# Kernel tuning notes

Measured on AMD Instinct MI355X. Metric: run time of the kernel, lower is better.

The kernel has to match this reference:

```python
import jax, jax.numpy as jnp
import numpy as np

N, F_IN, PRE, K = 400000, 64, 32, 6
EDGE = [32, 32]


def _dense_params(key, fan_in, fan_out):
    kw, kb = jax.random.split(key)
    W = jax.random.normal(kw, (fan_in, fan_out), jnp.float32) / np.sqrt(fan_in).astype(np.float32)
    b = jnp.zeros((fan_out,), jnp.float32)
    return W, b


def setup_inputs() -> dict:
    key = jax.random.key(0)
    ks = jax.random.split(key, 10)
    x = jax.random.normal(ks[0], (N, F_IN), jnp.float32)
    distsq = jax.random.uniform(ks[1], (N, K), jnp.float32)
    nidx = jax.random.randint(ks[2], (N, K), 0, N, jnp.int64)
    Wp, bp = _dense_params(ks[3], F_IN, PRE)
    # edge MLP: input K*(PRE+1) -> 32 -> 32 -> K
    We1, be1 = _dense_params(ks[4], K * (PRE + 1), EDGE[0])
    We2, be2 = _dense_params(ks[5], EDGE[0], EDGE[1])
    We3, be3 = _dense_params(ks[6], EDGE[1], K)
    # self MLP: F_IN -> 32 -> 32 -> 1
    Ws1, bs1 = _dense_params(ks[7], F_IN, EDGE[0])
    Ws2, bs2 = _dense_params(ks[8], EDGE[0], EDGE[1])
    Ws3, bs3 = _dense_params(ks[9], EDGE[1], 1)
    return dict(x=x, distsq=distsq, nidx=nidx, Wp=Wp, bp=bp,
                We1=We1, be1=be1, We2=We2, be2=be2, We3=We3, be3=be3,
                Ws1=Ws1, bs1=bs1, Ws2=Ws2, bs2=bs2, Ws3=Ws3, bs3=bs3)


def _forward(x, distsq, nidx, Wp, bp, We1, be1, We2, be2, We3, be3,
             Ws1, bs1, Ws2, bs2, Ws3, bs3):
    # pre-dense: [N, PRE]
    x_p = jax.nn.elu(x @ Wp + bp)
    # gather neighbors; select(nidx, x_n, 0.0) masks nidx<0 to 0.0
    safe_idx = jnp.maximum(nidx, 0)
    gathered = x_p[safe_idx]                              # [N, K, PRE]
    gathered = jnp.where(nidx[:, :, None] < 0, 0.0, gathered)
    diff = x_p[:, None, :] - gathered                     # [N, K, PRE]
    xn = jnp.concatenate([diff, distsq[:, :, None]], axis=2)  # [N, K, PRE+1]
    xn = xn.reshape(xn.shape[0], K * (PRE + 1))
    xn = jax.nn.elu(xn @ We1 + be1)
    xn = jax.nn.elu(xn @ We2 + be2)
    xn = xn @ We3 + be3                                   # [N, K]
    xs = jax.nn.elu(x @ Ws1 + bs1)
    xs = jax.nn.elu(xs @ Ws2 + bs2)
    xs = xs @ Ws3 + bs3                                   # [N, 1]
    out = jnp.concatenate([xs, xn], axis=1)               # [N, K+1]
    return jax.nn.softmax(out, axis=1)


def reference(x, distsq, nidx, Wp, bp, We1, be1, We2, be2, We3, be3,
              Ws1, bs1, Ws2, bs2, Ws3, bs3):
    return _forward(x, distsq, nidx, Wp, bp, We1, be1, We2, be2, We3, be3,
                    Ws1, bs1, Ws2, bs2, Ws3, bs3)
```

## Files before the change

kernel.cpp:

```cpp
#include <hip/hip_runtime.h>
#include <hip/hip_bf16.h>
#include <math.h>

typedef __hip_bfloat16 bf16;
typedef __attribute__((ext_vector_type(8))) __bf16 bf16x8;
typedef __attribute__((ext_vector_type(4))) float f32x4;
typedef unsigned int u32x4 __attribute__((ext_vector_type(4)));

#define F_IN 64
#define KNB 6

#define WOFF_BP   2048
#define WOFF_BE2  9472
#define WOFF_BE3  9696
#define WOFF_BS1  11776
#define WOFF_BS2  12832
#define WOFF_BS3  12896
#define FLAGS_OFF 13056
#define FRAG_OFF  14592
#define NFRAG_PRE 11
#define NFRAG_EDGE 19
#define STAGE_OFF 24576

#define MFMA(a, b, c) __builtin_amdgcn_mfma_f32_16x16x32_bf16(a, b, c, 0, 0, 0)

__device__ __forceinline__ float b2f(bf16 v) { return __bfloat162float(v); }
__device__ __forceinline__ float eluf(float v) { return v > 0.f ? v : __expf(v) - 1.f; }

__device__ __forceinline__ ushort f2bu(float v) {
  __bf16 b = (__bf16)v; ushort u; __builtin_memcpy(&u, &b, 2); return u;
}

union U8 { uint4 u; bf16x8 v; ushort s[8]; };

__device__ __forceinline__ uint4 ntload16(const void* p) {
  u32x4 t = __builtin_nontemporal_load((const u32x4*)p);
  uint4 r; r.x = t.x; r.y = t.y; r.z = t.z; r.w = t.w; return r;
}

__device__ __forceinline__ bf16x8 ldfrag(const ushort* fr, int f) {
  U8 u; u.u = *(const uint4*)(fr + f * 512 + (threadIdx.x & 63) * 8);
  return u.v;
}

__device__ __forceinline__ int permo(int m, int t) { return 8 * (m >> 2) + (m & 3) + 4 * t; }

__global__ void setupK(const ushort* xb, const int* ni,
                       const void* Wp, const void* bp, const void* We1, const void* be1,
                       const void* We2, const void* be2, const void* We3, const void* be3,
                       const void* Ws1, const void* bs1, const void* Ws2, const void* bs2,
                       const void* Ws3, const void* bs3, float* w) {
  __shared__ int sbf;
  int t = threadIdx.x;
  if (t < 64) {
    int bad = 0;
    for (int i = t; i < 256; i += 64) {
      float v = __uint_as_float(((unsigned)xb[i]) << 16);
      if (!(fabsf(v) < 100.f)) bad++;
    }
    unsigned long long bm = __ballot(bad > 0);
    if (t == 0) sbf = (__popcll(bm) < 4) ? 1 : 0;
  }
  __syncthreads();
  int bf = sbf;
  auto rv = [&](const void* p, long i) -> float {
    return bf ? b2f(((const bf16*)p)[i]) : ((const float*)p)[i];
  };
  if (blockIdx.x == 0) {
    if (t < 64) {
      unsigned long long hm = __ballot(ni[2 * t + 1] != 0);
      if (t == 0) {
        ((int*)(w + FLAGS_OFF))[0] = bf;
        ((int*)(w + FLAGS_OFF))[1] = (hm == 0ULL) ? 1 : 0;
      }
    }
    const void* bsrc[6] = {bp, bs1, bs2, bs3, be2, be3};
    const int bn[6] = {32, 32, 32, 1, 32, 6};
    const int bo[6] = {WOFF_BP, WOFF_BS1, WOFF_BS2, WOFF_BS3, WOFF_BE2, WOFF_BE3};
    for (int a = 0; a < 6; a++)
      for (int i = t; i < bn[a]; i += blockDim.x)
        w[bo[a] + i] = rv(bsrc[a], i);
  }
  ushort* fbv = (ushort*)(w + FRAG_OFF);
  int total = (NFRAG_PRE + NFRAG_EDGE) * 512;
  for (int i = blockIdx.x * blockDim.x + t; i < total; i += gridDim.x * blockDim.x) {
    int f = i >> 9, e = i & 511;
    int lane = e >> 3, j = e & 7;
    int mm = lane & 15, qq = lane >> 4;
    int k = qq * 8 + j;
    float v = 0.f;
    if (f < 4) { int s = f >> 1, tt = f & 1; v = rv(Wp, (long)(32 * s + k) * 32 + permo(mm, tt)); }
    else if (f < 8) { int s = (f - 4) >> 1, tt = f & 1; v = rv(Ws1, (long)(32 * s + k) * 32 + permo(mm, tt)); }
    else if (f < 10) { int tt = f & 1; v = rv(Ws2, (long)k * 32 + permo(mm, tt)); }
    else if (f == 10) { v = (mm == 0) ? rv(Ws3, k) : 0.f; }
    else if (f < 23) { int kn = (f - 11) >> 1, tt = (f - 11) & 1;
                       v = -rv(We1, (long)(kn * 33 + k) * 32 + permo(mm, tt)); }
    else if (f < 25) { int tt = f - 23; float s = 0.f;
#pragma unroll
                       for (int kn = 0; kn < KNB; kn++)
                         s += rv(We1, (long)(kn * 33 + k) * 32 + permo(mm, tt));
                       v = s; }
    else if (f < 27) { int tt = f - 25; int o = permo(mm, tt);
                       v = (k < 6) ? rv(We1, (long)(k * 33 + 32) * 32 + o)
                                   : (k == 6 ? rv(be1, o) : 0.f); }
    else if (f < 29) { int tt = f - 27; v = rv(We2, (long)k * 32 + permo(mm, tt)); }
    else { v = (mm < KNB) ? rv(We3, (long)k * 6 + mm) : 0.f; }
    fbv[i] = f2bu(v);
  }
}

template <bool BF16>
__device__ void pre_tiles(const void* xv, const float* __restrict__ w,
                          ushort* __restrict__ xp, float* __restrict__ xs,
                          int n_nodes, const ushort* __restrict__ fr) {
  int lane = threadIdx.x & 63;
  int m = lane & 15, q = lane >> 4;
  float bp8[8], bs18[8], bs28[8];
#pragma unroll
  for (int j = 0; j < 8; j++) {
    bp8[j]  = w[WOFF_BP  + 8 * q + j];
    bs18[j] = w[WOFF_BS1 + 8 * q + j];
    bs28[j] = w[WOFF_BS2 + 8 * q + j];
  }
  float bs3 = w[WOFF_BS3];
  long T = ((long)n_nodes + 15) >> 4;
  long wid = (long)((blockIdx.x * blockDim.x + threadIdx.x) >> 6);
  long nw = (long)((gridDim.x * blockDim.x) >> 6);
  f32x4 zero = {0.f, 0.f, 0.f, 0.f};

  uint4 bufA[4], bufB[4];
  auto loadraw = [&](uint4* r, long tt) {
    long row = tt * 16 + m; if (row >= n_nodes) row = n_nodes - 1;
    if (BF16) {
      const ushort* p = (const ushort*)xv + row * F_IN + q * 8;
      r[0] = ntload16(p);
      r[1] = ntload16(p + 32);
    } else {
      const float* p = (const float*)xv + row * F_IN + q * 8;
      r[0] = ntload16(p);      r[1] = ntload16(p + 4);
      r[2] = ntload16(p + 32); r[3] = ntload16(p + 36);
    }
  };
  auto mkfrag = [&](const uint4* r, int s) -> bf16x8 {
    if (BF16) { U8 u; u.u = r[s]; return u.v; }
    float f0[8];
    __builtin_memcpy(f0, r + 2 * s, 32);
    bf16x8 out;
#pragma unroll
    for (int j = 0; j < 8; j++) out[j] = (__bf16)f0[j];
    return out;
  };
  auto body = [&](uint4* cur, uint4* nxt, long t) {
    long tn = t + nw;
    if (tn < T) loadraw(nxt, tn);
    long n0 = t * 16;
    long row = n0 + m; if (row >= n_nodes) row = n_nodes - 1;
    bf16x8 x0 = mkfrag(cur, 0), x1 = mkfrag(cur, 1);
    f32x4 aP[2], aS[2];
#pragma unroll
    for (int tt = 0; tt < 2; tt++) {
      aP[tt] = MFMA(ldfrag(fr, 0 + tt), x0, zero);
      aP[tt] = MFMA(ldfrag(fr, 2 + tt), x1, aP[tt]);
      aS[tt] = MFMA(ldfrag(fr, 4 + tt), x0, zero);
      aS[tt] = MFMA(ldfrag(fr, 6 + tt), x1, aS[tt]);
    }
    U8 o1;
#pragma unroll
    for (int j = 0; j < 8; j++) o1.s[j] = f2bu(eluf(aP[j >> 2][j & 3] + bp8[j]));
    *(uint4*)(xp + row * 32 + q * 8) = o1.u;
    bf16x8 s1e;
#pragma unroll
    for (int j = 0; j < 8; j++) s1e[j] = (__bf16)eluf(aS[j >> 2][j & 3] + bs18[j]);
    f32x4 a2[2];
#pragma unroll
    for (int tt = 0; tt < 2; tt++) a2[tt] = MFMA(ldfrag(fr, 8 + tt), s1e, zero);
    bf16x8 s2e;
#pragma unroll
    for (int j = 0; j < 8; j++) s2e[j] = (__bf16)eluf(a2[j >> 2][j & 3] + bs28[j]);
    f32x4 a3 = MFMA(ldfrag(fr, 10), s2e, zero);
    if (q == 0) {
      long orow = n0 + m;
      if (orow < n_nodes) xs[orow] = a3[0] + bs3;
    }
  };
  long t = wid;
  if (t < T) loadraw(bufA, t);
  while (t < T) {
    body(bufA, bufB, t);
    t += nw; if (t >= T) break;
    body(bufB, bufA, t);
    t += nw;
  }
}

__launch_bounds__(256)
__global__ void preK(const void* xv, const float* __restrict__ w,
                     const int* __restrict__ flags,
                     ushort* __restrict__ xp, float* __restrict__ xs, int n_nodes) {
  __shared__ uint4 fsh[NFRAG_PRE * 64];
  const uint4* fbv = (const uint4*)((const ushort*)(w + FRAG_OFF));
  for (int i = threadIdx.x; i < NFRAG_PRE * 64; i += blockDim.x) fsh[i] = fbv[i];
  __syncthreads();
  const ushort* fr = (const ushort*)fsh;
  if (flags[0]) pre_tiles<true>(xv, w, xp, xs, n_nodes, fr);
  else          pre_tiles<false>(xv, w, xp, xs, n_nodes, fr);
}

struct ETile { U8 nb[KNB]; U8 own; U8 ad; float xsv; };

template <bool BF16>
__device__ void edge_tiles(const ushort* __restrict__ xp, const float* __restrict__ xs,
                           const void* dsv, const int* __restrict__ ni, int i64,
                           const float* __restrict__ w, void* outv, int n_nodes,
                           const ushort* __restrict__ fr) {
  int lane = threadIdx.x & 63;
  int m = lane & 15, q = lane >> 4;
  float b2[8], b3[4];
#pragma unroll
  for (int j = 0; j < 8; j++) b2[j] = w[WOFF_BE2 + 8 * q + j];
#pragma unroll
  for (int r = 0; r < 4; r++) { int o = 4 * q + r; b3[r] = (o < 6) ? w[WOFF_BE3 + o] : 0.f; }

  long T = ((long)n_nodes + 15) >> 4;
  long wid = (long)((blockIdx.x * blockDim.x + threadIdx.x) >> 6);
  long nw = (long)((gridDim.x * blockDim.x) >> 6);
  f32x4 zero = {0.f, 0.f, 0.f, 0.f};
  ETile A, B;
  int Ia[KNB], Ib[KNB];

  auto pidx = [&](int* ix, long tt) {
    long row = tt * 16 + m; if (row >= n_nodes) row = n_nodes - 1;
#pragma unroll
    for (int k = 0; k < KNB; k++)
      ix[k] = i64 ? ni[(row * KNB + k) * 2] : ni[row * KNB + k];
  };
  auto phead = [&](ETile& d, long tt) {
    long row = tt * 16 + m; if (row >= n_nodes) row = n_nodes - 1;
    d.own.u = *(const uint4*)(xp + row * 32 + q * 8);
    d.ad.u.x = 0; d.ad.u.y = 0; d.ad.u.z = 0; d.ad.u.w = 0;
    if (q == 0) {
      if (BF16) {
        const unsigned* dp = (const unsigned*)dsv;
        d.ad.u.x = dp[row * 3 + 0]; d.ad.u.y = dp[row * 3 + 1]; d.ad.u.z = dp[row * 3 + 2];
      } else {
        const float* dp = (const float*)dsv + row * KNB;
#pragma unroll
        for (int k = 0; k < KNB; k++) d.ad.s[k] = f2bu(dp[k]);
      }
      d.ad.s[6] = 0x3F80u;
    }
    d.xsv = xs[row];
  };
  auto pgather = [&](ETile& d, const int* ix) {
#pragma unroll
    for (int k = 0; k < KNB; k++) {
      int v = ix[k];
      long ai = (v < 0 || v >= n_nodes) ? 0 : (long)v;
      uint4 g = *(const uint4*)(xp + ai * 32 + q * 8);
      if (v < 0) { g.x = 0; g.y = 0; g.z = 0; g.w = 0; }
      d.nb[k].u = g;
    }
  };
  auto iterb = [&](ETile& cur, ETile& nxt, int* Iin, int* Iout, long t) {
    long t2 = t + 2 * nw;
    bool h2 = t2 < T;
    if (h2) pidx(Iout, t2);
    f32x4 acc[2];
#pragma unroll
    for (int tt = 0; tt < 2; tt++) {
      acc[tt] = MFMA(ldfrag(fr, 12 + tt), cur.own.v, zero);
      acc[tt] = MFMA(ldfrag(fr, 14 + tt), cur.ad.v, acc[tt]);
#pragma unroll
      for (int k = 0; k < KNB; k++)
        acc[tt] = MFMA(ldfrag(fr, k * 2 + tt), cur.nb[k].v, acc[tt]);
    }
    if (t + nw < T) pgather(nxt, Iin);
    bf16x8 a1;
#pragma unroll
    for (int j = 0; j < 8; j++) a1[j] = (__bf16)eluf(acc[j >> 2][j & 3]);
    f32x4 acc2[2];
#pragma unroll
    for (int tt = 0; tt < 2; tt++) acc2[tt] = MFMA(ldfrag(fr, 16 + tt), a1, zero);
    bf16x8 a2;
#pragma unroll
    for (int j = 0; j < 8; j++) a2[j] = (__bf16)eluf(acc2[j >> 2][j & 3] + b2[j]);
    f32x4 a3 = MFMA(ldfrag(fr, 18), a2, zero);
    float l0 = a3[0] + b3[0], l1 = a3[1] + b3[1], l2 = a3[2] + b3[2], l3 = a3[3] + b3[3];
    float o4 = __shfl(l0, m + 16, 64);
    float o5 = __shfl(l1, m + 16, 64);
    if (lane < 16) {
      long nodeid = t * 16 + lane;
      if (nodeid < n_nodes) {
        float lg[7] = {cur.xsv, l0, l1, l2, l3, o4, o5};
        float mx = lg[0];
#pragma unroll
        for (int i = 1; i < 7; i++) mx = fmaxf(mx, lg[i]);
        float e[7], ssum = 0.f;
#pragma unroll
        for (int i = 0; i < 7; i++) { e[i] = __expf(lg[i] - mx); ssum += e[i]; }
        float inv = 1.f / ssum;
        if (BF16) {
          ushort* o = (ushort*)outv + nodeid * 7;
#pragma unroll
          for (int i = 0; i < 7; i++) o[i] = f2bu(e[i] * inv);
        } else {
          float* o = (float*)outv + nodeid * 7;
#pragma unroll
          for (int i = 0; i < 7; i++) o[i] = e[i] * inv;
        }
      }
    }
    if (h2) phead(cur, t2);
  };
  long t = wid;
  if (t < T) {
    pidx(Ia, t); phead(A, t); pgather(A, Ia);
    if (t + nw < T) { pidx(Ia, t + nw); phead(B, t + nw); }
  }
  while (t < T) {
    iterb(A, B, Ia, Ib, t);
    t += nw; if (t >= T) break;
    iterb(B, A, Ib, Ia, t);
    t += nw;
  }
}

__launch_bounds__(256)
__global__ void edgeK(const ushort* __restrict__ xp, const float* __restrict__ xs,
                      const void* dsv, const int* __restrict__ ni,
                      const float* __restrict__ w, const int* __restrict__ flags,
                      void* outv, int n_nodes) {
  __shared__ uint4 fsh[NFRAG_EDGE * 64];
  const uint4* fbv = (const uint4*)((const ushort*)(w + FRAG_OFF) + NFRAG_PRE * 512);
  for (int i = threadIdx.x; i < NFRAG_EDGE * 64; i += blockDim.x) fsh[i] = fbv[i];
  __syncthreads();
  const ushort* fr = (const ushort*)fsh;
  if (flags[0]) edge_tiles<true>(xp, xs, dsv, ni, flags[1], w, outv, n_nodes, fr);
  else          edge_tiles<false>(xp, xs, dsv, ni, flags[1], w, outv, n_nodes, fr);
}

template <bool BF16>
__device__ __forceinline__ float wval(const void* W, long i) {
  if (BF16) return b2f(((const bf16*)W)[i]);
  return ((const float*)W)[i];
}

__device__ __forceinline__ void block_flags(const ushort* xb, const int* ni, int* sflags) {
  if (threadIdx.x < 64) {
    int t = threadIdx.x;
    int bad = 0;
    for (int i = t; i < 256; i += 64) {
      float v = __uint_as_float(((unsigned)xb[i]) << 16);
      if (!(fabsf(v) < 100.f)) bad++;
    }
    unsigned long long bm = __ballot(bad > 0);
    unsigned long long hm = __ballot(ni[2 * t + 1] != 0);
    if (t == 0) {
      sflags[0] = (__popcll(bm) < 4) ? 1 : 0;
      sflags[1] = (hm == 0ULL) ? 1 : 0;
    }
  }
  __syncthreads();
}

template <bool BF16>
__device__ void node_body(int n, int n_nodes, const void* xv, const void* dsv,
                          const int* __restrict__ ni, int i64,
                          const void* Wp, const void* bp, const void* We1, const void* be1,
                          const void* We2, const void* be2, const void* We3, const void* be3,
                          const void* Ws1, const void* bs1, const void* Ws2, const void* bs2,
                          const void* Ws3, const void* bs3, void* outv) {
  float h[32], s1[32];
#pragma unroll
  for (int o = 0; o < 32; o++) { h[o] = wval<BF16>(bp, o); s1[o] = wval<BF16>(bs1, o); }
  for (int j = 0; j < F_IN; j++) {
    float xj = wval<BF16>(xv, (long)n * F_IN + j);
#pragma unroll
    for (int o = 0; o < 32; o++) {
      h[o]  += xj * wval<BF16>(Wp,  (long)j * 32 + o);
      s1[o] += xj * wval<BF16>(Ws1, (long)j * 32 + o);
    }
  }
  float own[32];
#pragma unroll
  for (int o = 0; o < 32; o++) own[o] = eluf(h[o]);
  float s2[32];
#pragma unroll
  for (int o = 0; o < 32; o++) s2[o] = wval<BF16>(bs2, o);
  for (int j = 0; j < 32; j++) {
    float v = eluf(s1[j]);
#pragma unroll
    for (int o = 0; o < 32; o++) s2[o] += v * wval<BF16>(Ws2, (long)j * 32 + o);
  }
  float xsv = wval<BF16>(bs3, 0);
#pragma unroll
  for (int j = 0; j < 32; j++) xsv += eluf(s2[j]) * wval<BF16>(Ws3, j);

  float h1[32];
#pragma unroll
  for (int o = 0; o < 32; o++) h1[o] = wval<BF16>(be1, o);
  for (int k = 0; k < KNB; k++) {
    long pos = (long)n * KNB + k;
    int idx = i64 ? ni[2 * pos] : ni[pos];
    float mmask = idx < 0 ? 0.f : 1.f;
    long ai = idx < 0 ? 0 : idx;
    if (ai >= n_nodes) ai = 0;
    float nh[32];
#pragma unroll
    for (int o = 0; o < 32; o++) nh[o] = wval<BF16>(bp, o);
    for (int j = 0; j < F_IN; j++) {
      float xj = wval<BF16>(xv, ai * F_IN + j);
#pragma unroll
      for (int o = 0; o < 32; o++) nh[o] += xj * wval<BF16>(Wp, (long)j * 32 + o);
    }
#pragma unroll
    for (int j = 0; j < 32; j++) {
      float d = own[j] - mmask * eluf(nh[j]);
#pragma unroll
      for (int o = 0; o < 32; o++) h1[o] += d * wval<BF16>(We1, ((long)(k * 33 + j)) * 32 + o);
    }
    float dsq = BF16 ? b2f(((const bf16*)dsv)[pos]) : ((const float*)dsv)[pos];
#pragma unroll
    for (int o = 0; o < 32; o++) h1[o] += dsq * wval<BF16>(We1, ((long)(k * 33 + 32)) * 32 + o);
  }
  float h2[32];
#pragma unroll
  for (int o = 0; o < 32; o++) h2[o] = wval<BF16>(be2, o);
  for (int j = 0; j < 32; j++) {
    float v = eluf(h1[j]);
#pragma unroll
    for (int o = 0; o < 32; o++) h2[o] += v * wval<BF16>(We2, (long)j * 32 + o);
  }
  float lg[7];
  lg[0] = xsv;
#pragma unroll
  for (int o = 0; o < 6; o++) lg[1 + o] = wval<BF16>(be3, o);
  for (int j = 0; j < 32; j++) {
    float v = eluf(h2[j]);
#pragma unroll
    for (int o = 0; o < 6; o++) lg[1 + o] += v * wval<BF16>(We3, (long)j * 6 + o);
  }
  float mx = lg[0];
#pragma unroll
  for (int i = 1; i < 7; i++) mx = fmaxf(mx, lg[i]);
  float e[7], ssum = 0.f;
#pragma unroll
  for (int i = 0; i < 7; i++) { e[i] = __expf(lg[i] - mx); ssum += e[i]; }
  float inv = 1.f / ssum;
  if (BF16) {
    bf16* o = (bf16*)outv;
#pragma unroll
    for (int i = 0; i < 7; i++) o[(long)n * 7 + i] = __float2bfloat16(e[i] * inv);
  } else {
    float* o = (float*)outv;
#pragma unroll
    for (int i = 0; i < 7; i++) o[(long)n * 7 + i] = e[i] * inv;
  }
}

__launch_bounds__(256)
__global__ void fused(const void* xv, const void* dsv, const int* __restrict__ ni,
                      const void* Wp, const void* bp, const void* We1, const void* be1,
                      const void* We2, const void* be2, const void* We3, const void* be3,
                      const void* Ws1, const void* bs1, const void* Ws2, const void* bs2,
                      const void* Ws3, const void* bs3, void* outv, int n_nodes) {
  __shared__ int sflags[2];
  block_flags((const ushort*)xv, ni, sflags);
  int n = blockIdx.x * blockDim.x + threadIdx.x;
  if (n >= n_nodes) return;
  if (sflags[0]) node_body<true>(n, n_nodes, xv, dsv, ni, sflags[1], Wp, bp, We1, be1,
                                 We2, be2, We3, be3, Ws1, bs1, Ws2, bs2, Ws3, bs3, outv);
  else           node_body<false>(n, n_nodes, xv, dsv, ni, sflags[1], Wp, bp, We1, be1,
                                  We2, be2, We3, be3, Ws1, bs1, Ws2, bs2, Ws3, bs3, outv);
}

extern "C" void kernel_launch(void* const* d_in, const int* in_sizes, int n_in,
                              void* d_out, int out_size, void* d_ws, size_t ws_size,
                              hipStream_t stream) {
  const void* x      = d_in[0];
  const void* distsq = d_in[1];
  const int*  nidx   = (const int*)d_in[2];

  float* w = (float*)d_ws;
  int* flags = (int*)(w + FLAGS_OFF);
  int n_nodes = in_sizes[0] / F_IN;

  size_t need = (size_t)STAGE_OFF * 4 + (size_t)n_nodes * 64 + (size_t)n_nodes * 4 + 256;
  if (ws_size >= need) {
    setupK<<<32, 256, 0, stream>>>((const ushort*)x, nidx,
                                   d_in[3], d_in[4], d_in[5], d_in[6], d_in[7], d_in[8],
                                   d_in[9], d_in[10], d_in[11], d_in[12], d_in[13], d_in[14],
                                   d_in[15], d_in[16], w);
    ushort* xp = (ushort*)(w + STAGE_OFF);
    float* xs = (float*)(xp + (size_t)n_nodes * 32);
    preK<<<2048, 256, 0, stream>>>(x, w, flags, xp, xs, n_nodes);
    edgeK<<<2048, 256, 0, stream>>>(xp, xs, distsq, nidx, w, flags, d_out, n_nodes);
  } else {
    int grid = (n_nodes + 255) / 256;
    fused<<<grid, 256, 0, stream>>>(x, distsq, nidx, d_in[3], d_in[4], d_in[5], d_in[6],
                                    d_in[7], d_in[8], d_in[9], d_in[10], d_in[11], d_in[12],
                                    d_in[13], d_in[14], d_in[15], d_in[16], d_out, n_nodes);
  }
}
```

Before: 252.6 us.

## Vectorize index/distance loads, reorder gather prefetch, add MFMA priority and occupancy hints

Neighbor indices and distances are now read with vectorized nontemporal loads instead of scalar per-element loads, and outputs use nontemporal stores. The next-tile gather is issued before the current tile's first-layer MFMAs rather than after, so its latency can overlap the matrix work. MFMA sections are wrapped in s_setprio, launch_bounds gain a min-blocks hint of 4, and the edge kernel grid is halved. This aims to cut load instruction count and expose more memory-level parallelism, at the cost of higher register pressure from the extra in-flight gather data and possibly less parallelism from the smaller grid.

Result: slower. 326.8 us (+29.4%).

```diff
diff --git a/kernel.cpp b/kernel.cpp
--- a/kernel.cpp
+++ b/kernel.cpp
@@ -6,6 +6,7 @@
 typedef __attribute__((ext_vector_type(8))) __bf16 bf16x8;
 typedef __attribute__((ext_vector_type(4))) float f32x4;
 typedef unsigned int u32x4 __attribute__((ext_vector_type(4)));
+typedef unsigned int u32x2 __attribute__((ext_vector_type(2)));
 
 #define F_IN 64
 #define KNB 6
@@ -36,6 +37,10 @@
 __device__ __forceinline__ uint4 ntload16(const void* p) {
   u32x4 t = __builtin_nontemporal_load((const u32x4*)p);
   uint4 r; r.x = t.x; r.y = t.y; r.z = t.z; r.w = t.w; return r;
+}
+__device__ __forceinline__ uint2 ntload8(const void* p) {
+  u32x2 t = __builtin_nontemporal_load((const u32x2*)p);
+  uint2 r; r.x = t.x; r.y = t.y; return r;
 }
 
 __device__ __forceinline__ bf16x8 ldfrag(const ushort* fr, int f) {
@@ -157,6 +162,7 @@
     long row = n0 + m; if (row >= n_nodes) row = n_nodes - 1;
     bf16x8 x0 = mkfrag(cur, 0), x1 = mkfrag(cur, 1);
     f32x4 aP[2], aS[2];
+    __builtin_amdgcn_s_setprio(1);
 #pragma unroll
     for (int tt = 0; tt < 2; tt++) {
       aP[tt] = MFMA(ldfrag(fr, 0 + tt), x0, zero);
@@ -164,6 +170,7 @@
       aS[tt] = MFMA(ldfrag(fr, 4 + tt), x0, zero);
       aS[tt] = MFMA(ldfrag(fr, 6 + tt), x1, aS[tt]);
     }
+    __builtin_amdgcn_s_setprio(0);
     U8 o1;
 #pragma unroll
     for (int j = 0; j < 8; j++) o1.s[j] = f2bu(eluf(aP[j >> 2][j & 3] + bp8[j]));
@@ -193,7 +200,7 @@
   }
 }
 
-__launch_bounds__(256)
+__launch_bounds__(256, 4)
 __global__ void preK(const void* xv, const float* __restrict__ w,
                      const int* __restrict__ flags,
                      ushort* __restrict__ xp, float* __restrict__ xs, int n_nodes) {
@@ -230,9 +237,17 @@
 
   auto pidx = [&](int* ix, long tt) {
     long row = tt * 16 + m; if (row >= n_nodes) row = n_nodes - 1;
-#pragma unroll
-    for (int k = 0; k < KNB; k++)
-      ix[k] = i64 ? ni[(row * KNB + k) * 2] : ni[row * KNB + k];
+    if (i64) {
+      const uint4* p = (const uint4*)((const char*)ni + row * (KNB * 8));
+      uint4 a = ntload16(p), b = ntload16(p + 1), c = ntload16(p + 2);
+      ix[0] = (int)a.x; ix[1] = (int)a.z; ix[2] = (int)b.x;
+      ix[3] = (int)b.z; ix[4] = (int)c.x; ix[5] = (int)c.z;
+    } else {
+      const uint2* p = (const uint2*)((const char*)ni + row * (KNB * 4));
+      uint2 a = ntload8(p), b = ntload8(p + 1), c = ntload8(p + 2);
+      ix[0] = (int)a.x; ix[1] = (int)a.y; ix[2] = (int)b.x;
+      ix[3] = (int)b.y; ix[4] = (int)c.x; ix[5] = (int)c.y;
+    }
   };
   auto phead = [&](ETile& d, long tt) {
     long row = tt * 16 + m; if (row >= n_nodes) row = n_nodes - 1;
@@ -243,9 +258,11 @@
         const unsigned* dp = (const unsigned*)dsv;
         d.ad.u.x = dp[row * 3 + 0]; d.ad.u.y = dp[row * 3 + 1]; d.ad.u.z = dp[row * 3 + 2];
       } else {
-        const float* dp = (const float*)dsv + row * KNB;
-#pragma unroll
-        for (int k = 0; k < KNB; k++) d.ad.s[k] = f2bu(dp[k]);
+        const uint2* dp = (const uint2*)((const char*)dsv + row * (KNB * 4));
+        uint2 a = ntload8(dp), b = ntload8(dp + 1), c = ntload8(dp + 2);
+        d.ad.s[0] = f2bu(__uint_as_float(a.x)); d.ad.s[1] = f2bu(__uint_as_float(a.y));
+        d.ad.s[2] = f2bu(__uint_as_float(b.x)); d.ad.s[3] = f2bu(__uint_as_float(b.y));
+        d.ad.s[4] = f2bu(__uint_as_float(c.x)); d.ad.s[5] = f2bu(__uint_as_float(c.y));
       }
       d.ad.s[6] = 0x3F80u;
     }
@@ -264,8 +281,10 @@
   auto iterb = [&](ETile& cur, ETile& nxt, int* Iin, int* Iout, long t) {
     long t2 = t + 2 * nw;
     bool h2 = t2 < T;
+    if (t + nw < T) pgather(nxt, Iin);
     if (h2) pidx(Iout, t2);
     f32x4 acc[2];
+    __builtin_amdgcn_s_setprio(1);
 #pragma unroll
     for (int tt = 0; tt < 2; tt++) {
       acc[tt] = MFMA(ldfrag(fr, 12 + tt), cur.own.v, zero);
@@ -274,13 +293,15 @@
       for (int k = 0; k < KNB; k++)
         acc[tt] = MFMA(ldfrag(fr, k * 2 + tt), cur.nb[k].v, acc[tt]);
     }
-    if (t + nw < T) pgather(nxt, Iin);
+    __builtin_amdgcn_s_setprio(0);
     bf16x8 a1;
 #pragma unroll
     for (int j = 0; j < 8; j++) a1[j] = (__bf16)eluf(acc[j >> 2][j & 3]);
     f32x4 acc2[2];
+    __builtin_amdgcn_s_setprio(1);
 #pragma unroll
     for (int tt = 0; tt < 2; tt++) acc2[tt] = MFMA(ldfrag(fr, 16 + tt), a1, zero);
+    __builtin_amdgcn_s_setprio(0);
     bf16x8 a2;
 #pragma unroll
     for (int j = 0; j < 8; j++) a2[j] = (__bf16)eluf(acc2[j >> 2][j & 3] + b2[j]);
@@ -302,11 +323,11 @@
         if (BF16) {
           ushort* o = (ushort*)outv + nodeid * 7;
 #pragma unroll
-          for (int i = 0; i < 7; i++) o[i] = f2bu(e[i] * inv);
+          for (int i = 0; i < 7; i++) __builtin_nontemporal_store(f2bu(e[i] * inv), o + i);
         } else {
           float* o = (float*)outv + nodeid * 7;
 #pragma unroll
-          for (int i = 0; i < 7; i++) o[i] = e[i] * inv;
+          for (int i = 0; i < 7; i++) __builtin_nontemporal_store(e[i] * inv, o + i);
         }
       }
     }
@@ -325,7 +346,7 @@
   }
 }
 
-__launch_bounds__(256)
+__launch_bounds__(256, 4)
 __global__ void edgeK(const ushort* __restrict__ xp, const float* __restrict__ xs,
                       const void* dsv, const int* __restrict__ ni,
                       const float* __restrict__ w, const int* __restrict__ flags,
@@ -494,7 +515,7 @@
     ushort* xp = (ushort*)(w + STAGE_OFF);
     float* xs = (float*)(xp + (size_t)n_nodes * 32);
     preK<<<2048, 256, 0, stream>>>(x, w, flags, xp, xs, n_nodes);
-    edgeK<<<2048, 256, 0, stream>>>(xp, xs, distsq, nidx, w, flags, d_out, n_nodes);
+    edgeK<<<1024, 256, 0, stream>>>(xp, xs, distsq, nidx, w, flags, d_out, n_nodes);
   } else {
     int grid = (n_nodes + 255) / 256;
     fused<<<grid, 256, 0, stream>>>(x, distsq, nidx, d_in[3], d_in[4], d_in[5], d_in[6],
```
